# Kernel tuning notes

Measured on AMD Instinct MI355X. Metric: run time of the kernel, lower is better.

The kernel has to match this reference:

```python
import jax, jax.numpy as jnp
import numpy as np
import math

D = 512      # input_size == hidden_size
TAU = 4      # length of att/spatial lists
N = 16384    # tokens (batch*H*W)

def setup_inputs() -> dict:
    key = jax.random.key(0)
    ks = jax.random.split(key, 16)
    s = 1.0 / math.sqrt(D)
    return {
        "T_t": jax.random.normal(ks[0], (N, D), jnp.float32),
        "S_t": jax.random.normal(ks[1], (N, D), jnp.float32),
        "t_att": jax.random.normal(ks[2], (TAU, N, D), jnp.float32),
        "s_att": jax.random.normal(ks[3], (TAU, N, D), jnp.float32),
        "t_spatial": jax.random.normal(ks[4], (TAU, N, D), jnp.float32),
        "s_spatial": jax.random.normal(ks[5], (TAU, N, D), jnp.float32),
        # fl_t: Linear(D, 3D); fl_t_next: Linear(D, D); same for s
        "W_t": jax.random.uniform(ks[6], (3 * D, D), jnp.float32, -s, s),
        "b_t": jax.random.uniform(ks[7], (3 * D,), jnp.float32, -s, s),
        "W_tn": jax.random.uniform(ks[8], (D, D), jnp.float32, -s, s),
        "b_tn": jax.random.uniform(ks[9], (D,), jnp.float32, -s, s),
        "W_s": jax.random.uniform(ks[10], (3 * D, D), jnp.float32, -s, s),
        "b_s": jax.random.uniform(ks[11], (3 * D,), jnp.float32, -s, s),
        "W_sn": jax.random.uniform(ks[12], (D, D), jnp.float32, -s, s),
        "b_sn": jax.random.uniform(ks[13], (D,), jnp.float32, -s, s),
    }

def reference(T_t, S_t, t_att, s_att, t_spatial, s_spatial,
              W_t, b_t, W_tn, b_tn, W_s, b_s, W_sn, b_sn):
    d = T_t.shape[-1]
    scale = 1.0 / jnp.sqrt(jnp.asarray(d, T_t.dtype))
    s_next = S_t @ W_sn.T + b_sn          # [N, D]
    t_next = T_t @ W_tn.T + b_tn          # [N, D]

    # trend weights: dot-product along feature dim, softmax over tau axis
    w_s = jax.nn.softmax(jnp.einsum('knd,nd->kn', s_att, s_next) * scale, axis=0)
    w_t = jax.nn.softmax(jnp.einsum('knd,nd->kn', t_spatial, t_next) * scale, axis=0)
    T_trend = jnp.einsum('knd,kn->nd', t_att, w_s)      # [N, D]
    S_trend = jnp.einsum('knd,kn->nd', s_spatial, w_t)  # [N, D]

    t_gate = jax.nn.sigmoid(t_next)
    s_gate = jax.nn.sigmoid(s_next)
    T_fusion = T_t * t_gate + (1.0 - t_gate) * T_trend
    S_fusion = S_t * s_gate + (1.0 - s_gate) * S_trend

    T_concat = T_fusion @ W_t.T + b_t     # [N, 3D]
    S_concat = S_fusion @ W_s.T + b_s
    t_g, t_t, t_s = jnp.split(T_concat, 3, axis=1)
    s_g, s_t, s_s = jnp.split(S_concat, 3, axis=1)
    T_gate = jax.nn.sigmoid(t_g)
    S_gate = jax.nn.sigmoid(s_g)
    T_new = T_gate * t_t + (1.0 - T_gate) * s_t
    S_new = S_gate * s_s + (1.0 - S_gate) * t_s
    return T_new, S_new
```

## Files before the change

kernel.cpp:

```cpp
#include <hip/hip_runtime.h>

#define NTOK 16384
#define DIM 512
#define NTAU 4

typedef __attribute__((ext_vector_type(4))) float f32x4;
typedef __attribute__((ext_vector_type(8))) short bf16x8;
typedef __attribute__((ext_vector_type(4))) unsigned short u16x4;
typedef __attribute__((ext_vector_type(8))) unsigned short u16x8;
typedef unsigned int u32;

__device__ inline unsigned short f2bf(float f) {
    union { float f; unsigned int u; } v; v.f = f;
    unsigned int u = v.u + 0x7FFFu + ((v.u >> 16) & 1u);
    return (unsigned short)(u >> 16);
}

__device__ inline void bf8_to_f32(u16x8 h, f32x4& a, f32x4& b) {
    union { unsigned int u; float f; } t;
#pragma unroll
    for (int e = 0; e < 4; e++) { t.u = ((unsigned int)h[e]) << 16; a[e] = t.f; }
#pragma unroll
    for (int e = 0; e < 4; e++) { t.u = ((unsigned int)h[4 + e]) << 16; b[e] = t.f; }
}

#define NTLOAD4(p) __builtin_nontemporal_load((const f32x4*)(p))

__device__ __forceinline__ void gload16(const void* g, void* l) {
    __builtin_amdgcn_global_load_lds((const __attribute__((address_space(1))) u32*)g,
                                     (__attribute__((address_space(3))) u32*)l, 16, 0, 0);
}

__global__ void convert_all(const float* __restrict__ a, const float* __restrict__ b,
                            const float* __restrict__ c, const float* __restrict__ d,
                            unsigned short* __restrict__ oa, unsigned short* __restrict__ ob,
                            unsigned short* __restrict__ oc, unsigned short* __restrict__ od) {
    int i = blockIdx.x * 256 + threadIdx.x;
    const float* s; unsigned short* t; int off;
    if (i < 65536)       { s = a; t = oa; off = i; }
    else if (i < 131072) { s = b; t = ob; off = i - 65536; }
    else if (i < 327680) { s = c; t = oc; off = i - 131072; }
    else                 { s = d; t = od; off = i - 327680; }
    f32x4 v = ((const f32x4*)s)[off];
    u16x4 o;
    o[0] = f2bf(v[0]); o[1] = f2bf(v[1]); o[2] = f2bf(v[2]); o[3] = f2bf(v[3]);
    ((u16x4*)t)[off] = o;
}

__global__ __launch_bounds__(256, 2) void gemm_next2(
    const float* __restrict__ T_t, const float* __restrict__ S_t,
    const unsigned short* __restrict__ Wtn, const unsigned short* __restrict__ Wsn,
    const float* __restrict__ btn, const float* __restrict__ bsn,
    unsigned short* __restrict__ t_next, unsigned short* __restrict__ s_next)
{
    __shared__ unsigned short lA[128][40];
    __shared__ unsigned short lB[128][40];
    const int tid = threadIdx.x;
    const int id = blockIdx.x;
    const int xcd = id & 7;
    const int rest = id >> 3;
    const int mat = rest & 1;
    const int idx = rest >> 1;
    const float* A = mat ? S_t : T_t;
    const unsigned short* W = mat ? Wsn : Wtn;
    const float* bias = mat ? bsn : btn;
    unsigned short* out = mat ? s_next : t_next;
    const int m0 = (xcd * 16 + (idx >> 2)) * 128;
    const int n0 = (idx & 3) * 128;
    const int lane = tid & 63;
    const int w = tid >> 6;
    const int wr = w >> 1, wc = w & 1;

    f32x4 acc[4][4];
#pragma unroll
    for (int i = 0; i < 4; i++)
#pragma unroll
        for (int j = 0; j < 4; j++) acc[i][j] = (f32x4){0.f, 0.f, 0.f, 0.f};

    const int arow = tid >> 3;
    const int acol = (tid & 7) * 4;
    const int brow = tid >> 2;
    const int bcol = (tid & 3) * 8;

    for (int k0 = 0; k0 < DIM; k0 += 32) {
#pragma unroll
        for (int i = 0; i < 4; i++) {
            int r = arow + 32 * i;
            f32x4 v = *(const f32x4*)(A + (size_t)(m0 + r) * DIM + k0 + acol);
            u16x4 o;
            o[0] = f2bf(v[0]); o[1] = f2bf(v[1]); o[2] = f2bf(v[2]); o[3] = f2bf(v[3]);
            *(u16x4*)&lA[r][acol] = o;
        }
#pragma unroll
        for (int i = 0; i < 2; i++) {
            int r = brow + 64 * i;
            u16x8 v = *(const u16x8*)(W + (size_t)(n0 + r) * DIM + k0 + bcol);
            *(u16x8*)&lB[r][bcol] = v;
        }
        __syncthreads();

        bf16x8 af[4], bfr[4];
#pragma unroll
        for (int i = 0; i < 4; i++)
            af[i] = *(const bf16x8*)&lA[wr * 64 + i * 16 + (lane & 15)][(lane >> 4) * 8];
#pragma unroll
        for (int j = 0; j < 4; j++)
            bfr[j] = *(const bf16x8*)&lB[wc * 64 + j * 16 + (lane & 15)][(lane >> 4) * 8];
#pragma unroll
        for (int i = 0; i < 4; i++)
#pragma unroll
            for (int j = 0; j < 4; j++)
                acc[i][j] = __builtin_amdgcn_mfma_f32_16x16x32_bf16(af[i], bfr[j], acc[i][j], 0, 0, 0);
        __syncthreads();
    }

#pragma unroll
    for (int j = 0; j < 4; j++) {
        int n = n0 + wc * 64 + j * 16 + (lane & 15);
        float bv = bias[n];
#pragma unroll
        for (int i = 0; i < 4; i++) {
            int mbase = m0 + wr * 64 + i * 16 + (lane >> 4) * 4;
#pragma unroll
            for (int r = 0; r < 4; r++)
                out[(size_t)(mbase + r) * DIM + n] = f2bf(acc[i][j][r] + bv);
        }
    }
}

__global__ __launch_bounds__(256) void dots_kernel(
    const float* __restrict__ s_att, const float* __restrict__ t_spatial,
    const unsigned short* __restrict__ t_next, const unsigned short* __restrict__ s_next,
    float* __restrict__ w_all)
{
    const int lane = threadIdx.x & 63;
    const int n = (blockIdx.x << 2) + (threadIdx.x >> 6);
    const int c = lane * 8;
    const size_t rb = (size_t)n * DIM + c;
    const float scale = 0.04419417382415922f;

    f32x4 tn_a, tn_b, sn_a, sn_b;
    bf8_to_f32(*(const u16x8*)(t_next + rb), tn_a, tn_b);
    bf8_to_f32(*(const u16x8*)(s_next + rb), sn_a, sn_b);

    float dws[NTAU], dwt[NTAU];
#pragma unroll
    for (int k = 0; k < NTAU; k++) {
        const size_t kb = ((size_t)k * NTOK + n) * DIM + c;
        f32x4 a0 = NTLOAD4(s_att + kb);
        f32x4 a1 = NTLOAD4(s_att + kb + 4);
        f32x4 b0 = NTLOAD4(t_spatial + kb);
        f32x4 b1 = NTLOAD4(t_spatial + kb + 4);
        dws[k] = a0[0]*sn_a[0]+a0[1]*sn_a[1]+a0[2]*sn_a[2]+a0[3]*sn_a[3]
               + a1[0]*sn_b[0]+a1[1]*sn_b[1]+a1[2]*sn_b[2]+a1[3]*sn_b[3];
        dwt[k] = b0[0]*tn_a[0]+b0[1]*tn_a[1]+b0[2]*tn_a[2]+b0[3]*tn_a[3]
               + b1[0]*tn_b[0]+b1[1]*tn_b[1]+b1[2]*tn_b[2]+b1[3]*tn_b[3];
    }
#pragma unroll
    for (int k = 0; k < NTAU; k++) {
        float v = dws[k];
#pragma unroll
        for (int off = 32; off; off >>= 1) v += __shfl_xor(v, off);
        dws[k] = v * scale;
        float u = dwt[k];
#pragma unroll
        for (int off = 32; off; off >>= 1) u += __shfl_xor(u, off);
        dwt[k] = u * scale;
    }

    float ms = fmaxf(fmaxf(dws[0], dws[1]), fmaxf(dws[2], dws[3]));
    float mt = fmaxf(fmaxf(dwt[0], dwt[1]), fmaxf(dwt[2], dwt[3]));
    f32x4 wsv, wtv;
    float ssum = 0.f, tsum = 0.f;
#pragma unroll
    for (int k = 0; k < NTAU; k++) {
        wsv[k] = __expf(dws[k] - ms); ssum += wsv[k];
        wtv[k] = __expf(dwt[k] - mt); tsum += wtv[k];
    }
    float rs = 1.f / ssum, rt = 1.f / tsum;
#pragma unroll
    for (int k = 0; k < NTAU; k++) { wsv[k] *= rs; wtv[k] *= rt; }

    if (lane == 0) {
        *(f32x4*)(w_all + (size_t)n * 8)     = wsv;
        *(f32x4*)(w_all + (size_t)n * 8 + 4) = wtv;
    }
}

__global__ __launch_bounds__(256) void fusion_kernel(
    const float* __restrict__ T_t, const float* __restrict__ S_t,
    const float* __restrict__ t_att, const float* __restrict__ s_spatial,
    const unsigned short* __restrict__ t_next, const unsigned short* __restrict__ s_next,
    const float* __restrict__ w_all,
    unsigned short* __restrict__ Tf, unsigned short* __restrict__ Sf)
{
    const int lane = threadIdx.x & 63;
    const int n = (blockIdx.x << 2) + (threadIdx.x >> 6);
    const int c = lane * 8;
    const size_t rb = (size_t)n * DIM + c;

    f32x4 wsv = *(const f32x4*)(w_all + (size_t)n * 8);
    f32x4 wtv = *(const f32x4*)(w_all + (size_t)n * 8 + 4);

    f32x4 Tta = {0,0,0,0}, Ttb = {0,0,0,0}, Sta = {0,0,0,0}, Stb = {0,0,0,0};
#pragma unroll
    for (int k = 0; k < NTAU; k++) {
        const size_t kb = ((size_t)k * NTOK + n) * DIM + c;
        f32x4 ta = NTLOAD4(t_att + kb);
        f32x4 tb = NTLOAD4(t_att + kb + 4);
        f32x4 sa = NTLOAD4(s_spatial + kb);
        f32x4 sb = NTLOAD4(s_spatial + kb + 4);
        float wk = wsv[k], vk = wtv[k];
#pragma unroll
        for (int e = 0; e < 4; e++) {
            Tta[e] += wk * ta[e]; Ttb[e] += wk * tb[e];
            Sta[e] += vk * sa[e]; Stb[e] += vk * sb[e];
        }
    }

    f32x4 tn_a, tn_b, sn_a, sn_b;
    bf8_to_f32(*(const u16x8*)(t_next + rb), tn_a, tn_b);
    bf8_to_f32(*(const u16x8*)(s_next + rb), sn_a, sn_b);
    f32x4 Ta = NTLOAD4(T_t + rb);
    f32x4 Tb = NTLOAD4(T_t + rb + 4);
    f32x4 Sa = NTLOAD4(S_t + rb);
    f32x4 Sb = NTLOAD4(S_t + rb + 4);

    u16x8 oT, oS;
#pragma unroll
    for (int e = 0; e < 4; e++) {
        float gt_a = 1.f / (1.f + __expf(-tn_a[e]));
        float gt_b = 1.f / (1.f + __expf(-tn_b[e]));
        float gs_a = 1.f / (1.f + __expf(-sn_a[e]));
        float gs_b = 1.f / (1.f + __expf(-sn_b[e]));
        oT[e]     = f2bf(Ta[e] * gt_a + (1.f - gt_a) * Tta[e]);
        oT[4 + e] = f2bf(Tb[e] * gt_b + (1.f - gt_b) * Ttb[e]);
        oS[e]     = f2bf(Sa[e] * gs_a + (1.f - gs_a) * Sta[e]);
        oS[4 + e] = f2bf(Sb[e] * gs_b + (1.f - gs_b) * Stb[e]);
    }
    *(u16x8*)(Tf + rb) = oT;
    *(u16x8*)(Sf + rb) = oS;
}

__global__ __launch_bounds__(256, 2) void gemm_final(
    const unsigned short* __restrict__ Tf, const unsigned short* __restrict__ Sf,
    const unsigned short* __restrict__ Wt, const unsigned short* __restrict__ Ws,
    const float* __restrict__ bt, const float* __restrict__ bs,
    float* __restrict__ out)
{
    __shared__ __align__(16) unsigned short lT[2][128][32];
    __shared__ __align__(16) unsigned short lS[2][128][32];
    __shared__ __align__(16) unsigned short lW[2][384][32];
    const int tid = threadIdx.x;
    const int id = blockIdx.x + 8 * blockIdx.y;
    const int xcd = id & 7;
    const int idx = id >> 3;
    const int m0 = (xcd * 16 + (idx >> 3)) * 128;
    const int j0 = (idx & 7) * 64;
    const int lane = tid & 63;
    const int w = tid >> 6, wr = w >> 1, wc = w & 1;

    f32x4 acc[6][4][2];
#pragma unroll
    for (int g = 0; g < 6; g++)
#pragma unroll
        for (int i = 0; i < 4; i++)
#pragma unroll
            for (int jj = 0; jj < 2; jj++) acc[g][i][jj] = (f32x4){0.f, 0.f, 0.f, 0.f};

    const int srow = lane >> 2;
    const int sg   = lane & 3;

    auto stageW = [&](int buf, int k0, int rbase) {
        const int r = rbase + srow;
        const int lg = sg ^ ((r >> 1) & 3);
        const int g = r >> 6;
        const unsigned short* src = (g < 3) ? Wt : Ws;
        const int wrow = (g < 3 ? g : g - 3) * DIM + j0 + (r & 63);
        gload16(src + (size_t)wrow * DIM + k0 + lg * 8, &lW[buf][rbase][0]);
    };
    auto stage = [&](int buf, int kt) {
        const int k0 = kt * 32;
        if (w < 2) {
            const int rbs = w * 64;
#pragma unroll
            for (int i = 0; i < 4; i++) {
                const int row = rbs + i * 16 + srow;
                const int lg = sg ^ ((row >> 1) & 3);
                gload16(Tf + (size_t)(m0 + row) * DIM + k0 + lg * 8, &lT[buf][rbs + i * 16][0]);
                gload16(Sf + (size_t)(m0 + row) * DIM + k0 + lg * 8, &lS[buf][rbs + i * 16][0]);
            }
            stageW(buf, k0, w * 32);
            stageW(buf, k0, w * 32 + 16);
        } else {
            const int rbs = 64 + (w - 2) * 160;
#pragma unroll
            for (int i = 0; i < 10; i++)
                stageW(buf, k0, rbs + i * 16);
        }
    };

    stage(0, 0);
    __syncthreads();

    int cur = 0;
    for (int kt = 0; kt < 16; ++kt) {
        if (kt < 15) stage(cur ^ 1, kt + 1);

        bf16x8 aT[4], aS[4];
#pragma unroll
        for (int i = 0; i < 4; i++) {
            const int row = wr * 64 + i * 16 + (lane & 15);
            const int pg = (lane >> 4) ^ ((row >> 1) & 3);
            aT[i] = *(const bf16x8*)&lT[cur][row][pg * 8];
            aS[i] = *(const bf16x8*)&lS[cur][row][pg * 8];
        }
#pragma unroll
        for (int g = 0; g < 6; g++) {
#pragma unroll
            for (int jj = 0; jj < 2; jj++) {
                const int r = g * 64 + wc * 32 + jj * 16 + (lane & 15);
                const int pg = (lane >> 4) ^ ((r >> 1) & 3);
                bf16x8 bw = *(const bf16x8*)&lW[cur][r][pg * 8];
#pragma unroll
                for (int i = 0; i < 4; i++)
                    acc[g][i][jj] = __builtin_amdgcn_mfma_f32_16x16x32_bf16(
                        (g < 3) ? aT[i] : aS[i], bw, acc[g][i][jj], 0, 0, 0);
            }
        }
        __syncthreads();
        cur ^= 1;
    }

#pragma unroll
    for (int jj = 0; jj < 2; jj++) {
        const int j = j0 + wc * 32 + jj * 16 + (lane & 15);
        const float btg = bt[j], btt = bt[512 + j], bts = bt[1024 + j];
        const float bsg = bs[j], bst = bs[512 + j], bss = bs[1024 + j];
#pragma unroll
        for (int i = 0; i < 4; i++) {
            int mbase = m0 + wr * 64 + i * 16 + (lane >> 4) * 4;
#pragma unroll
            for (int r = 0; r < 4; r++) {
                float TG = acc[0][i][jj][r] + btg;
                float TT = acc[1][i][jj][r] + btt;
                float TS = acc[2][i][jj][r] + bts;
                float SG = acc[3][i][jj][r] + bsg;
                float ST = acc[4][i][jj][r] + bst;
                float SS = acc[5][i][jj][r] + bss;
                float gT = 1.f / (1.f + __expf(-TG));
                float gS = 1.f / (1.f + __expf(-SG));
                size_t m = (size_t)(mbase + r);
                out[m * DIM + j] = gT * TT + (1.f - gT) * ST;
                out[(size_t)NTOK * DIM + m * DIM + j] = gS * SS + (1.f - gS) * TS;
            }
        }
    }
}

extern "C" void kernel_launch(void* const* d_in, const int* in_sizes, int n_in,
                              void* d_out, int out_size, void* d_ws, size_t ws_size,
                              hipStream_t stream) {
    const float* T_t       = (const float*)d_in[0];
    const float* S_t       = (const float*)d_in[1];
    const float* t_att     = (const float*)d_in[2];
    const float* s_att     = (const float*)d_in[3];
    const float* t_spatial = (const float*)d_in[4];
    const float* s_spatial = (const float*)d_in[5];
    const float* W_t  = (const float*)d_in[6];
    const float* b_t  = (const float*)d_in[7];
    const float* W_tn = (const float*)d_in[8];
    const float* b_tn = (const float*)d_in[9];
    const float* W_s  = (const float*)d_in[10];
    const float* b_s  = (const float*)d_in[11];
    const float* W_sn = (const float*)d_in[12];
    const float* b_sn = (const float*)d_in[13];
    float* out = (float*)d_out;

    char* ws = (char*)d_ws;
    unsigned short* t_next = (unsigned short*)(ws + 0);
    unsigned short* s_next = (unsigned short*)(ws + 16777216);
    unsigned short* Tf     = (unsigned short*)(ws + 33554432);
    unsigned short* Sf     = (unsigned short*)(ws + 50331648);
    unsigned short* Wtn_b  = (unsigned short*)(ws + 67108864);
    unsigned short* Wsn_b  = (unsigned short*)(ws + 67633152);
    unsigned short* Wt_b   = (unsigned short*)(ws + 68157440);
    unsigned short* Ws_b   = (unsigned short*)(ws + 69730304);
    float*          w_all  = (float*)(ws + 71303168);

    convert_all<<<2048, 256, 0, stream>>>(W_tn, W_sn, W_t, W_s,
                                          Wtn_b, Wsn_b, Wt_b, Ws_b);

    gemm_next2<<<1024, 256, 0, stream>>>(T_t, S_t, Wtn_b, Wsn_b, b_tn, b_sn,
                                         t_next, s_next);

    dots_kernel<<<4096, 256, 0, stream>>>(s_att, t_spatial, t_next, s_next, w_all);

    fusion_kernel<<<4096, 256, 0, stream>>>(T_t, S_t, t_att, s_spatial,
                                            t_next, s_next, w_all, Tf, Sf);

    dim3 g3(8, 128);
    gemm_final<<<g3, 256, 0, stream>>>(Tf, Sf, Wt_b, Ws_b, b_t, b_s, out);
}
```

Measured before the change: 307.3 us.

## Widen final GEMM to 512 threads and remap token blocks per XCD

The final fused GEMM now runs with 8 waves per block instead of 4. Each wave covers a 16-column slice rather than 32, which halves the accumulator registers per wave, and staging is spread evenly across all waves. The dots and fusion kernels remap block indices so each XCD handles a contiguous range of tokens, aiming for better L2 locality on t_next/s_next and the weights. The trade-offs are more redundant LDS reads of the A fragments per wave and heavier barrier synchronization across 8 waves.

```diff
diff --git a/kernel.cpp b/kernel.cpp
--- a/kernel.cpp
+++ b/kernel.cpp
@@ -134,7 +134,8 @@
     float* __restrict__ w_all)
 {
     const int lane = threadIdx.x & 63;
-    const int n = (blockIdx.x << 2) + (threadIdx.x >> 6);
+    const int id = blockIdx.x;
+    const int n = (id & 7) * 2048 + (id >> 3) * 4 + (threadIdx.x >> 6);
     const int c = lane * 8;
     const size_t rb = (size_t)n * DIM + c;
     const float scale = 0.04419417382415922f;
@@ -195,7 +196,8 @@
     unsigned short* __restrict__ Tf, unsigned short* __restrict__ Sf)
 {
     const int lane = threadIdx.x & 63;
-    const int n = (blockIdx.x << 2) + (threadIdx.x >> 6);
+    const int id = blockIdx.x;
+    const int n = (id & 7) * 2048 + (id >> 3) * 4 + (threadIdx.x >> 6);
     const int c = lane * 8;
     const size_t rb = (size_t)n * DIM + c;
 
@@ -242,7 +244,7 @@
     *(u16x8*)(Sf + rb) = oS;
 }
 
-__global__ __launch_bounds__(256, 2) void gemm_final(
+__global__ __launch_bounds__(512, 2) void gemm_final(
     const unsigned short* __restrict__ Tf, const unsigned short* __restrict__ Sf,
     const unsigned short* __restrict__ Wt, const unsigned short* __restrict__ Ws,
     const float* __restrict__ bt, const float* __restrict__ bs,
@@ -252,51 +254,47 @@
     __shared__ __align__(16) unsigned short lS[2][128][32];
     __shared__ __align__(16) unsigned short lW[2][384][32];
     const int tid = threadIdx.x;
-    const int id = blockIdx.x + 8 * blockIdx.y;
+    const int id = blockIdx.x;
     const int xcd = id & 7;
     const int idx = id >> 3;
     const int m0 = (xcd * 16 + (idx >> 3)) * 128;
     const int j0 = (idx & 7) * 64;
     const int lane = tid & 63;
-    const int w = tid >> 6, wr = w >> 1, wc = w & 1;
-
-    f32x4 acc[6][4][2];
+    const int w = tid >> 6;
+    const int wr = w & 1;
+    const int wjc = w >> 1;
+
+    f32x4 acc[6][4];
 #pragma unroll
     for (int g = 0; g < 6; g++)
 #pragma unroll
-        for (int i = 0; i < 4; i++)
-#pragma unroll
-            for (int jj = 0; jj < 2; jj++) acc[g][i][jj] = (f32x4){0.f, 0.f, 0.f, 0.f};
+        for (int i = 0; i < 4; i++) acc[g][i] = (f32x4){0.f, 0.f, 0.f, 0.f};
 
     const int srow = lane >> 2;
     const int sg   = lane & 3;
 
-    auto stageW = [&](int buf, int k0, int rbase) {
-        const int r = rbase + srow;
-        const int lg = sg ^ ((r >> 1) & 3);
-        const int g = r >> 6;
-        const unsigned short* src = (g < 3) ? Wt : Ws;
-        const int wrow = (g < 3 ? g : g - 3) * DIM + j0 + (r & 63);
-        gload16(src + (size_t)wrow * DIM + k0 + lg * 8, &lW[buf][rbase][0]);
-    };
     auto stage = [&](int buf, int kt) {
         const int k0 = kt * 32;
-        if (w < 2) {
-            const int rbs = w * 64;
-#pragma unroll
-            for (int i = 0; i < 4; i++) {
-                const int row = rbs + i * 16 + srow;
+#pragma unroll
+        for (int i = 0; i < 5; i++) {
+            const int ch = w * 5 + i;
+            if (ch < 8) {
+                const int row = ch * 16 + srow;
                 const int lg = sg ^ ((row >> 1) & 3);
-                gload16(Tf + (size_t)(m0 + row) * DIM + k0 + lg * 8, &lT[buf][rbs + i * 16][0]);
-                gload16(Sf + (size_t)(m0 + row) * DIM + k0 + lg * 8, &lS[buf][rbs + i * 16][0]);
+                gload16(Tf + (size_t)(m0 + row) * DIM + k0 + lg * 8, &lT[buf][ch * 16][0]);
+            } else if (ch < 16) {
+                const int row = (ch - 8) * 16 + srow;
+                const int lg = sg ^ ((row >> 1) & 3);
+                gload16(Sf + (size_t)(m0 + row) * DIM + k0 + lg * 8, &lS[buf][(ch - 8) * 16][0]);
+            } else {
+                const int rb = (ch - 16) * 16;
+                const int r = rb + srow;
+                const int lg = sg ^ ((r >> 1) & 3);
+                const int g = r >> 6;
+                const unsigned short* src = (g < 3) ? Wt : Ws;
+                const int wrow = (g < 3 ? g : g - 3) * DIM + j0 + (r & 63);
+                gload16(src + (size_t)wrow * DIM + k0 + lg * 8, &lW[buf][rb][0]);
             }
-            stageW(buf, k0, w * 32);
-            stageW(buf, k0, w * 32 + 16);
-        } else {
-            const int rbs = 64 + (w - 2) * 160;
-#pragma unroll
-            for (int i = 0; i < 10; i++)
-                stageW(buf, k0, rbs + i * 16);
         }
     };
 
@@ -317,43 +315,37 @@
         }
 #pragma unroll
         for (int g = 0; g < 6; g++) {
-#pragma unroll
-            for (int jj = 0; jj < 2; jj++) {
-                const int r = g * 64 + wc * 32 + jj * 16 + (lane & 15);
-                const int pg = (lane >> 4) ^ ((r >> 1) & 3);
-                bf16x8 bw = *(const bf16x8*)&lW[cur][r][pg * 8];
-#pragma unroll
-                for (int i = 0; i < 4; i++)
-                    acc[g][i][jj] = __builtin_amdgcn_mfma_f32_16x16x32_bf16(
-                        (g < 3) ? aT[i] : aS[i], bw, acc[g][i][jj], 0, 0, 0);
-            }
+            const int r = g * 64 + wjc * 16 + (lane & 15);
+            const int pg = (lane >> 4) ^ ((r >> 1) & 3);
+            bf16x8 bw = *(const bf16x8*)&lW[cur][r][pg * 8];
+#pragma unroll
+            for (int i = 0; i < 4; i++)
+                acc[g][i] = __builtin_amdgcn_mfma_f32_16x16x32_bf16(
+                    (g < 3) ? aT[i] : aS[i], bw, acc[g][i], 0, 0, 0);
         }
         __syncthreads();
         cur ^= 1;
     }
 
-#pragma unroll
-    for (int jj = 0; jj < 2; jj++) {
-        const int j = j0 + wc * 32 + jj * 16 + (lane & 15);
-        const float btg = bt[j], btt = bt[512 + j], bts = bt[1024 + j];
-        const float bsg = bs[j], bst = bs[512 + j], bss = bs[1024 + j];
-#pragma unroll
-        for (int i = 0; i < 4; i++) {
-            int mbase = m0 + wr * 64 + i * 16 + (lane >> 4) * 4;
-#pragma unroll
-            for (int r = 0; r < 4; r++) {
-                float TG = acc[0][i][jj][r] + btg;
-                float TT = acc[1][i][jj][r] + btt;
-                float TS = acc[2][i][jj][r] + bts;
-                float SG = acc[3][i][jj][r] + bsg;
-                float ST = acc[4][i][jj][r] + bst;
-                float SS = acc[5][i][jj][r] + bss;
-                float gT = 1.f / (1.f + __expf(-TG));
-                float gS = 1.f / (1.f + __expf(-SG));
-                size_t m = (size_t)(mbase + r);
-                out[m * DIM + j] = gT * TT + (1.f - gT) * ST;
-                out[(size_t)NTOK * DIM + m * DIM + j] = gS * SS + (1.f - gS) * TS;
-            }
+    const int j = j0 + wjc * 16 + (lane & 15);
+    const float btg = bt[j], btt = bt[512 + j], bts = bt[1024 + j];
+    const float bsg = bs[j], bst = bs[512 + j], bss = bs[1024 + j];
+#pragma unroll
+    for (int i = 0; i < 4; i++) {
+        int mbase = m0 + wr * 64 + i * 16 + (lane >> 4) * 4;
+#pragma unroll
+        for (int r = 0; r < 4; r++) {
+            float TG = acc[0][i][r] + btg;
+            float TT = acc[1][i][r] + btt;
+            float TS = acc[2][i][r] + bts;
+            float SG = acc[3][i][r] + bsg;
+            float ST = acc[4][i][r] + bst;
+            float SS = acc[5][i][r] + bss;
+            float gT = 1.f / (1.f + __expf(-TG));
+            float gS = 1.f / (1.f + __expf(-SG));
+            size_t m = (size_t)(mbase + r);
+            out[m * DIM + j] = gT * TT + (1.f - gT) * ST;
+            out[(size_t)NTOK * DIM + m * DIM + j] = gS * SS + (1.f - gS) * TS;
         }
     }
 }
@@ -399,6 +391,5 @@
     fusion_kernel<<<4096, 256, 0, stream>>>(T_t, S_t, t_att, s_spatial,
                                             t_next, s_next, w_all, Tf, Sf);
 
-    dim3 g3(8, 128);
-    gemm_final<<<g3, 256, 0, stream>>>(Tf, Sf, Wt_b, Ws_b, b_t, b_s, out);
-}
+    gemm_final<<<1024, 512, 0, stream>>>(Tf, Sf, Wt_b, Ws_b, b_t, b_s, out);
+}
```

Result: faster. 289.0 us (-6.0%).
